# Kernel tuning notes

Hardware: AMD Instinct MI355X
Metric: run time of the kernel (lower is better)

The kernel has to match this reference:

```python
import jax, jax.numpy as jnp
import numpy as np

K = 5      # kernel_size
STRIDE = 1
EPS = 1e-7


def _extract_patches(x, k, s):
    # x: [B,H,W,C] -> [B,Ho,Wo,k,k,C], same (kh,kw,c) layout as tf.extract_image_patches VALID
    B, H, W, C = x.shape
    Ho = (H - k) // s + 1
    Wo = (W - k) // s + 1
    r = (jnp.arange(Ho) * s)[:, None] + jnp.arange(k)   # [Ho,k]
    c = (jnp.arange(Wo) * s)[:, None] + jnp.arange(k)   # [Wo,k]
    return x[:, r[:, None, :, None], c[None, :, None, :], :]


def _rotate(pflat, angle, k):
    # Replicates tf.contrib.image.transform with angles_to_projective_transforms,
    # including the (1+1e-7) normalization of the 3x3 matrix in the original code.
    # pflat: [N, k*k, C], angle: [N]; bilinear sampling, fill value 0 outside.
    N = pflat.shape[0]
    f32 = pflat.dtype
    co, si = jnp.cos(angle), jnp.sin(angle)
    km1 = jnp.asarray(k - 1, f32)
    xoff = (km1 - (co * km1 - si * km1)) * 0.5
    yoff = (km1 - (si * km1 + co * km1)) * 0.5
    scale = 1.0 / (1.0 + EPS)  # transforms /= transforms[:, 8:9] + 1e-7
    gy, gx = jnp.meshgrid(jnp.arange(k, dtype=f32), jnp.arange(k, dtype=f32), indexing='ij')
    sx = (co[:, None, None] * gx - si[:, None, None] * gy + xoff[:, None, None]) * scale
    sy = (si[:, None, None] * gx + co[:, None, None] * gy + yoff[:, None, None]) * scale
    sx = sx.reshape(N, k * k)
    sy = sy.reshape(N, k * k)
    x0 = jnp.floor(sx)
    y0 = jnp.floor(sy)
    wx = (sx - x0)[..., None]
    wy = (sy - y0)[..., None]
    x0i = x0.astype(jnp.int32)
    y0i = y0.astype(jnp.int32)

    def samp(yi, xi):
        valid = (xi >= 0) & (xi < k) & (yi >= 0) & (yi < k)
        idx = jnp.clip(yi, 0, k - 1) * k + jnp.clip(xi, 0, k - 1)   # [N,k*k]
        v = jnp.take_along_axis(pflat, idx[..., None], axis=1)      # [N,k*k,C]
        return jnp.where(valid[..., None], v, jnp.zeros((), f32))

    v00 = samp(y0i, x0i)
    v01 = samp(y0i, x0i + 1)
    v10 = samp(y0i + 1, x0i)
    v11 = samp(y0i + 1, x0i + 1)
    top = v00 * (1 - wx) + v01 * wx
    bot = v10 * (1 - wx) + v11 * wx
    return top * (1 - wy) + bot * wy   # [N,k*k,C]


def _forward(input_tensor, W, b):
    k, s = K, STRIDE
    B, H, Wd, C = input_tensor.shape
    patches = _extract_patches(input_tensor, k, s)      # [B,Ho,Wo,k,k,C]
    Ho, Wo = patches.shape[1], patches.shape[2]
    inten = patches.sum(-1)                             # [B,Ho,Wo,k,k] channel-sum intensity
    ridx = jnp.arange(k, dtype=patches.dtype)
    tot = inten.sum((-2, -1)) + EPS
    cr = (inten * ridx[:, None]).sum((-2, -1)) / tot    # centroid row
    cc = (inten * ridx[None, :]).sum((-2, -1)) / tot    # centroid col
    m = (k - 1) / 2.0                                   # meanCenter (same for row/col)
    angle = jnp.arctan2(cr - m, cc - m + EPS)           # [B,Ho,Wo]
    pflat = patches.reshape(B * Ho * Wo, k * k, C)
    rot = _rotate(pflat, angle.reshape(-1), k)          # [N,k*k,C]
    rot = rot.reshape(B, Ho * Wo, k * k * C)
    wflat = W.reshape(W.shape[0], -1)                   # [F, k*k*C]
    out = jnp.einsum('bpd,fd->bpf', rot, wflat)         # elementwise-mult-sum 'conv'
    return out.reshape(B, Ho, Wo, -1) + b


def setup_inputs():
    key = jax.random.key(0)
    k1, k2 = jax.random.split(key, 2)
    B, H, Wd, C, F = 4, 128, 128, 16, 32
    input_tensor = jax.random.uniform(k1, (B, H, Wd, C), dtype=jnp.float32)
    lim = float(np.sqrt(6.0 / (K * K * C + F)))  # glorot_uniform
    W = jax.random.uniform(k2, (F, K, K, C), minval=-lim, maxval=lim, dtype=jnp.float32)
    b = jnp.zeros((F,), jnp.float32)
    return {"input_tensor": input_tensor, "W": W, "b": b}


def reference(input_tensor, W, b):
    return _forward(input_tensor, W, b)
```

## Files before the change

### kernel.cpp

```cpp
#include <hip/hip_runtime.h>


#define KS     5
#define TILE   8
#define NPIX   64
#define TW     (TILE + KS - 1)
#define CPAD   20
#define C_IN   16
#define F_OUT  32
#define H_IN   128
#define W_IN   128
#define HO     124
#define WO     124
#define NBATCH 4
#define EPSF   1e-7f
#define BLOCK  256
#define NCHUNK 7
#define AROW   72
#define KW     400

typedef __attribute__((ext_vector_type(8))) short  short8;
typedef __attribute__((ext_vector_type(4))) float  floatx4;

static __device__ __forceinline__ short f2bf(float f) {
    union { float f; unsigned u; } v; v.f = f;
    unsigned r = v.u + 0x7fffu + ((v.u >> 16) & 1u);
    return (short)(r >> 16);
}

__global__ __launch_bounds__(BLOCK) void rotconv_kernel(
    const float* __restrict__ in, const float* __restrict__ Wg,
    const float* __restrict__ bg, float* __restrict__ out)
{
    __shared__ float s_in[TW * TW * CPAD];
    __shared__ float s_int[TW * (TW + 1)];
    __shared__ short sA[NPIX * AROW];

    const int tid  = threadIdx.x;
    const int bx = blockIdx.x, by = blockIdx.y, bimg = blockIdx.z;
    const int ox = bx * TILE, oy = by * TILE;

    const float* inb = in + (size_t)bimg * (H_IN * W_IN * C_IN);
    for (int i = tid; i < TW * TW * (C_IN / 4); i += BLOCK) {
        int cv = i & 3;
        int pp = i >> 2;
        int x = pp % TW, y = pp / TW;
        int gy = oy + y, gx = ox + x;
        float4 v = make_float4(0.f, 0.f, 0.f, 0.f);
        if (gy < H_IN && gx < W_IN)
            v = *(const float4*)(inb + ((size_t)(gy * W_IN + gx) * C_IN) + 4 * cv);
        *(float4*)(&s_in[pp * CPAD + 4 * cv]) = v;
    }
    __syncthreads();

    for (int pp = tid; pp < TW * TW; pp += BLOCK) {
        const float* sp = &s_in[pp * CPAD];
        float s = 0.f;
        #pragma unroll
        for (int c = 0; c < C_IN; ++c) s += sp[c];
        s_int[(pp / TW) * (TW + 1) + (pp % TW)] = s;
    }
    __syncthreads();

    const int p    = tid & 63;
    const int wv   = tid >> 6;
    const int lx   = p & 7, ly = p >> 3;
    const int col  = p & 15;
    const int quad = p >> 4;

    float tot = EPSF, cr = 0.f, cc = 0.f;
    #pragma unroll
    for (int dy = 0; dy < KS; ++dy)
        #pragma unroll
        for (int dx = 0; dx < KS; ++dx) {
            float v = s_int[(ly + dy) * (TW + 1) + (lx + dx)];
            tot += v; cr += v * (float)dy; cc += v * (float)dx;
        }
    cr /= tot; cc /= tot;
    float ang = atan2f(cr - 2.0f, cc - 2.0f + EPSF);
    float si, co;
    sincosf(ang, &si, &co);
    const float scl = 1.0f / (1.0f + EPSF);
    float xoff = (4.0f - (co * 4.0f - si * 4.0f)) * 0.5f;
    float yoff = (4.0f - (si * 4.0f + co * 4.0f)) * 0.5f;

    const int nt  = wv >> 1;
    const int mt0 = (wv & 1) * 2;

    floatx4 acc0, acc1;
    {
        float bv = bg[nt * 16 + col];
        acc0 = (floatx4){bv, bv, bv, bv};
        acc1 = acc0;
    }

    for (int ch = 0; ch < NCHUNK; ++ch) {
        int t = 4 * ch + wv;
        short8 alo = {0,0,0,0,0,0,0,0}, ahi = {0,0,0,0,0,0,0,0};
        if (t < KS * KS) {
            int ky = t / KS, kx = t - KS * ky;
            float sx = (co * (float)kx - si * (float)ky + xoff) * scl;
            float sy = (si * (float)kx + co * (float)ky + yoff) * scl;
            float fx0 = floorf(sx), fy0 = floorf(sy);
            float wx = sx - fx0, wy = sy - fy0;
            int x0 = (int)fx0, y0 = (int)fy0;
            int x1 = x0 + 1, y1 = y0 + 1;
            float vx0 = (x0 >= 0 && x0 < KS) ? 1.f : 0.f;
            float vx1 = (x1 >= 0 && x1 < KS) ? 1.f : 0.f;
            float vy0 = (y0 >= 0 && y0 < KS) ? 1.f : 0.f;
            float vy1 = (y1 >= 0 && y1 < KS) ? 1.f : 0.f;
            float w00 = (1.f - wx) * (1.f - wy) * vx0 * vy0;
            float w01 = wx * (1.f - wy) * vx1 * vy0;
            float w10 = (1.f - wx) * wy * vx0 * vy1;
            float w11 = wx * wy * vx1 * vy1;
            int cx0 = min(max(x0, 0), KS - 1), cx1 = min(max(x1, 0), KS - 1);
            int cy0 = min(max(y0, 0), KS - 1), cy1 = min(max(y1, 0), KS - 1);
            const float* p00 = &s_in[((ly + cy0) * TW + (lx + cx0)) * CPAD];
            const float* p01 = &s_in[((ly + cy0) * TW + (lx + cx1)) * CPAD];
            const float* p10 = &s_in[((ly + cy1) * TW + (lx + cx0)) * CPAD];
            const float* p11 = &s_in[((ly + cy1) * TW + (lx + cx1)) * CPAD];
            float r[16];
            #pragma unroll
            for (int cv = 0; cv < 4; ++cv) {
                float4 a = *(const float4*)(p00 + 4 * cv);
                float4 b = *(const float4*)(p01 + 4 * cv);
                float4 c = *(const float4*)(p10 + 4 * cv);
                float4 d = *(const float4*)(p11 + 4 * cv);
                r[4*cv+0] = w00 * a.x + w01 * b.x + w10 * c.x + w11 * d.x;
                r[4*cv+1] = w00 * a.y + w01 * b.y + w10 * c.y + w11 * d.y;
                r[4*cv+2] = w00 * a.z + w01 * b.z + w10 * c.z + w11 * d.z;
                r[4*cv+3] = w00 * a.w + w01 * b.w + w10 * c.w + w11 * d.w;
            }
            alo = (short8){f2bf(r[0]), f2bf(r[1]), f2bf(r[2]), f2bf(r[3]),
                           f2bf(r[4]), f2bf(r[5]), f2bf(r[6]), f2bf(r[7])};
            ahi = (short8){f2bf(r[8]),  f2bf(r[9]),  f2bf(r[10]), f2bf(r[11]),
                           f2bf(r[12]), f2bf(r[13]), f2bf(r[14]), f2bf(r[15])};
        }
        __syncthreads();
        *(short8*)(&sA[p * AROW + wv * 16])     = alo;
        *(short8*)(&sA[p * AROW + wv * 16 + 8]) = ahi;
        __syncthreads();

        int nk = (ch == NCHUNK - 1) ? 1 : 2;
        for (int kk = 0; kk < nk; ++kk) {
            int kg = ch * 64 + kk * 32 + quad * 8;
            short8 bf = {0,0,0,0,0,0,0,0};
            if (kg + 8 <= KW) {
                const float* wp = Wg + (size_t)(nt * 16 + col) * KW + kg;
                float4 a = *(const float4*)(wp);
                float4 b = *(const float4*)(wp + 4);
                bf = (short8){f2bf(a.x), f2bf(a.y), f2bf(a.z), f2bf(a.w),
                              f2bf(b.x), f2bf(b.y), f2bf(b.z), f2bf(b.w)};
            }
            short8 a0 = *(const short8*)(&sA[(16 * mt0 + col) * AROW + kk * 32 + quad * 8]);
            short8 a1 = *(const short8*)(&sA[(16 * mt0 + 16 + col) * AROW + kk * 32 + quad * 8]);
            acc0 = __builtin_amdgcn_mfma_f32_16x16x32_bf16(a0, bf, acc0, 0, 0, 0);
            acc1 = __builtin_amdgcn_mfma_f32_16x16x32_bf16(a1, bf, acc1, 0, 0, 0);
        }
    }

    #pragma unroll
    for (int r = 0; r < 4; ++r) {
        int pix0 = 16 * mt0 + quad * 4 + r;
        int ho = oy + (pix0 >> 3), wo = ox + (pix0 & 7);
        if (ho < HO && wo < WO)
            out[(((size_t)bimg * HO + ho) * WO + wo) * F_OUT + nt * 16 + col] = acc0[r];
        int pix1 = pix0 + 16;
        ho = oy + (pix1 >> 3); wo = ox + (pix1 & 7);
        if (ho < HO && wo < WO)
            out[(((size_t)bimg * HO + ho) * WO + wo) * F_OUT + nt * 16 + col] = acc1[r];
    }
}

extern "C" void kernel_launch(void* const* d_in, const int* in_sizes, int n_in,
                              void* d_out, int out_size, void* d_ws, size_t ws_size,
                              hipStream_t stream) {
    const float* in = (const float*)d_in[0];
    const float* Wg = (const float*)d_in[1];
    const float* bg = (const float*)d_in[2];
    float* out      = (float*)d_out;
    dim3 grid((WO + TILE - 1) / TILE, (HO + TILE - 1) / TILE, NBATCH);
    rotconv_kernel<<<grid, dim3(BLOCK), 0, stream>>>(in, Wg, bg, out);
}
```

Before: 75.94 us.

## Split K across waves with register-built A fragments and LDS reduction

Each wave now handles a subset of the 25 kernel taps for all 64 pixels and both filter halves, building bf16 A fragments directly in registers by bilinear blending instead of staging them through shared memory. Per-pixel angles are computed once by one wave and shared. Partial accumulators from the four waves are reduced through LDS and written with vectorized float4 stores. This removes the per-chunk double barriers and the sA staging, but adds a cross-wave reduction, more accumulator registers, and some redundant blend work. The launch-bounds hint now requests two blocks per CU.

New measurement: 74.09 us. 1.02x faster.

```diff
diff --git a/kernel.cpp b/kernel.cpp
--- a/kernel.cpp
+++ b/kernel.cpp
@@ -3,7 +3,6 @@
 
 #define KS     5
 #define TILE   8
-#define NPIX   64
 #define TW     (TILE + KS - 1)
 #define CPAD   20
 #define C_IN   16
@@ -15,9 +14,12 @@
 #define NBATCH 4
 #define EPSF   1e-7f
 #define BLOCK  256
-#define NCHUNK 7
-#define AROW   72
 #define KW     400
+
+#define ANG_OFF     12160
+#define RED_STRIDE  34
+#define RED_WAVE    (64 * RED_STRIDE)
+#define SMEM_BYTES  34816
 
 typedef __attribute__((ext_vector_type(8))) short  short8;
 typedef __attribute__((ext_vector_type(4))) float  floatx4;
@@ -28,13 +30,57 @@
     return (short)(r >> 16);
 }
 
-__global__ __launch_bounds__(BLOCK) void rotconv_kernel(
+static __device__ __forceinline__ short8 blend8(
+    const float* __restrict__ s_in, int lxq, int lyq,
+    float co, float si, float xo, float yo, int t, int ch0)
+{
+    const float scl = 1.0f / (1.0f + EPSF);
+    int ky = t / KS, kx = t - KS * ky;
+    float sx = (co * (float)kx - si * (float)ky + xo) * scl;
+    float sy = (si * (float)kx + co * (float)ky + yo) * scl;
+    float fx0 = floorf(sx), fy0 = floorf(sy);
+    float wx = sx - fx0, wy = sy - fy0;
+    int x0 = (int)fx0, y0 = (int)fy0;
+    int x1 = x0 + 1, y1 = y0 + 1;
+    float vx0 = (x0 >= 0 && x0 < KS) ? 1.f : 0.f;
+    float vx1 = (x1 >= 0 && x1 < KS) ? 1.f : 0.f;
+    float vy0 = (y0 >= 0 && y0 < KS) ? 1.f : 0.f;
+    float vy1 = (y1 >= 0 && y1 < KS) ? 1.f : 0.f;
+    float w00 = (1.f - wx) * (1.f - wy) * vx0 * vy0;
+    float w01 = wx * (1.f - wy) * vx1 * vy0;
+    float w10 = (1.f - wx) * wy * vx0 * vy1;
+    float w11 = wx * wy * vx1 * vy1;
+    int cx0 = min(max(x0, 0), KS - 1), cx1 = min(max(x1, 0), KS - 1);
+    int cy0 = min(max(y0, 0), KS - 1), cy1 = min(max(y1, 0), KS - 1);
+    const float* p00 = &s_in[((lyq + cy0) * TW + (lxq + cx0)) * CPAD + ch0];
+    const float* p01 = &s_in[((lyq + cy0) * TW + (lxq + cx1)) * CPAD + ch0];
+    const float* p10 = &s_in[((lyq + cy1) * TW + (lxq + cx0)) * CPAD + ch0];
+    const float* p11 = &s_in[((lyq + cy1) * TW + (lxq + cx1)) * CPAD + ch0];
+    float r[8];
+    #pragma unroll
+    for (int cv = 0; cv < 2; ++cv) {
+        float4 a = *(const float4*)(p00 + 4 * cv);
+        float4 b = *(const float4*)(p01 + 4 * cv);
+        float4 c = *(const float4*)(p10 + 4 * cv);
+        float4 d = *(const float4*)(p11 + 4 * cv);
+        r[4*cv+0] = w00 * a.x + w01 * b.x + w10 * c.x + w11 * d.x;
+        r[4*cv+1] = w00 * a.y + w01 * b.y + w10 * c.y + w11 * d.y;
+        r[4*cv+2] = w00 * a.z + w01 * b.z + w10 * c.z + w11 * d.z;
+        r[4*cv+3] = w00 * a.w + w01 * b.w + w10 * c.w + w11 * d.w;
+    }
+    return (short8){f2bf(r[0]), f2bf(r[1]), f2bf(r[2]), f2bf(r[3]),
+                    f2bf(r[4]), f2bf(r[5]), f2bf(r[6]), f2bf(r[7])};
+}
+
+__global__ __launch_bounds__(BLOCK, 2) void rotconv_kernel(
     const float* __restrict__ in, const float* __restrict__ Wg,
     const float* __restrict__ bg, float* __restrict__ out)
 {
-    __shared__ float s_in[TW * TW * CPAD];
-    __shared__ float s_int[TW * (TW + 1)];
-    __shared__ short sA[NPIX * AROW];
+    __shared__ __align__(16) char smem[SMEM_BYTES];
+    float*  s_in   = (float*)smem;
+    float*  s_int  = (float*)(smem + 11520);
+    float4* s_ang4 = (float4*)(smem + ANG_OFF);
+    float*  red    = (float*)smem;
 
     const int tid  = threadIdx.x;
     const int bx = blockIdx.x, by = blockIdx.y, bimg = blockIdx.z;
@@ -62,113 +108,109 @@
     }
     __syncthreads();
 
+    if (tid < 64) {
+        const int alx = tid & 7, aly = tid >> 3;
+        float tot = EPSF, cr = 0.f, cc = 0.f;
+        #pragma unroll
+        for (int dy = 0; dy < KS; ++dy)
+            #pragma unroll
+            for (int dx = 0; dx < KS; ++dx) {
+                float v = s_int[(aly + dy) * (TW + 1) + (alx + dx)];
+                tot += v; cr += v * (float)dy; cc += v * (float)dx;
+            }
+        cr /= tot; cc /= tot;
+        float ang = atan2f(cr - 2.0f, cc - 2.0f + EPSF);
+        float si, co;
+        sincosf(ang, &si, &co);
+        float xoff = (4.0f - (co * 4.0f - si * 4.0f)) * 0.5f;
+        float yoff = (4.0f - (si * 4.0f + co * 4.0f)) * 0.5f;
+        s_ang4[tid] = make_float4(co, si, xoff, yoff);
+    }
+    __syncthreads();
+
     const int p    = tid & 63;
     const int wv   = tid >> 6;
-    const int lx   = p & 7, ly = p >> 3;
     const int col  = p & 15;
     const int quad = p >> 4;
 
-    float tot = EPSF, cr = 0.f, cc = 0.f;
-    #pragma unroll
-    for (int dy = 0; dy < KS; ++dy)
-        #pragma unroll
-        for (int dx = 0; dx < KS; ++dx) {
-            float v = s_int[(ly + dy) * (TW + 1) + (lx + dx)];
-            tot += v; cr += v * (float)dy; cc += v * (float)dx;
+    float4 angs[4];
+    #pragma unroll
+    for (int m = 0; m < 4; ++m) angs[m] = s_ang4[16 * m + col];
+
+    floatx4 acc[4][2];
+    #pragma unroll
+    for (int m = 0; m < 4; ++m) {
+        acc[m][0] = (floatx4){0.f, 0.f, 0.f, 0.f};
+        acc[m][1] = acc[m][0];
+    }
+
+    const int nstep = (wv == 0) ? 4 : 3;
+    const int lxq = col & 7, lyq0 = col >> 3;
+    const int ch0 = (quad & 1) * 8;
+    const short8 zero8 = {0,0,0,0,0,0,0,0};
+
+    #pragma unroll
+    for (int s = 0; s < 4; ++s) {
+        if (s < nstep) {
+            const int ta = wv + 8 * s;
+            const int tb = ta + 4;
+            const int tq = (quad < 2) ? ta : tb;
+
+            short8 bf0 = zero8, bf1 = zero8;
+            if (tq < KS * KS) {
+                const float* wp0 = Wg + (size_t)col * KW + tq * 16 + ch0;
+                float4 a = *(const float4*)(wp0);
+                float4 b = *(const float4*)(wp0 + 4);
+                bf0 = (short8){f2bf(a.x), f2bf(a.y), f2bf(a.z), f2bf(a.w),
+                               f2bf(b.x), f2bf(b.y), f2bf(b.z), f2bf(b.w)};
+                const float* wp1 = wp0 + (size_t)16 * KW;
+                float4 c = *(const float4*)(wp1);
+                float4 d = *(const float4*)(wp1 + 4);
+                bf1 = (short8){f2bf(c.x), f2bf(c.y), f2bf(c.z), f2bf(c.w),
+                               f2bf(d.x), f2bf(d.y), f2bf(d.z), f2bf(d.w)};
+            }
+
+            #pragma unroll
+            for (int m = 0; m < 4; ++m) {
+                short8 av = zero8;
+                if (tq < KS * KS)
+                    av = blend8(s_in, lxq, 2 * m + lyq0,
+                                angs[m].x, angs[m].y, angs[m].z, angs[m].w,
+                                tq, ch0);
+                acc[m][0] = __builtin_amdgcn_mfma_f32_16x16x32_bf16(av, bf0, acc[m][0], 0, 0, 0);
+                acc[m][1] = __builtin_amdgcn_mfma_f32_16x16x32_bf16(av, bf1, acc[m][1], 0, 0, 0);
+            }
         }
-    cr /= tot; cc /= tot;
-    float ang = atan2f(cr - 2.0f, cc - 2.0f + EPSF);
-    float si, co;
-    sincosf(ang, &si, &co);
-    const float scl = 1.0f / (1.0f + EPSF);
-    float xoff = (4.0f - (co * 4.0f - si * 4.0f)) * 0.5f;
-    float yoff = (4.0f - (si * 4.0f + co * 4.0f)) * 0.5f;
-
-    const int nt  = wv >> 1;
-    const int mt0 = (wv & 1) * 2;
-
-    floatx4 acc0, acc1;
-    {
-        float bv = bg[nt * 16 + col];
-        acc0 = (floatx4){bv, bv, bv, bv};
-        acc1 = acc0;
-    }
-
-    for (int ch = 0; ch < NCHUNK; ++ch) {
-        int t = 4 * ch + wv;
-        short8 alo = {0,0,0,0,0,0,0,0}, ahi = {0,0,0,0,0,0,0,0};
-        if (t < KS * KS) {
-            int ky = t / KS, kx = t - KS * ky;
-            float sx = (co * (float)kx - si * (float)ky + xoff) * scl;
-            float sy = (si * (float)kx + co * (float)ky + yoff) * scl;
-            float fx0 = floorf(sx), fy0 = floorf(sy);
-            float wx = sx - fx0, wy = sy - fy0;
-            int x0 = (int)fx0, y0 = (int)fy0;
-            int x1 = x0 + 1, y1 = y0 + 1;
-            float vx0 = (x0 >= 0 && x0 < KS) ? 1.f : 0.f;
-            float vx1 = (x1 >= 0 && x1 < KS) ? 1.f : 0.f;
-            float vy0 = (y0 >= 0 && y0 < KS) ? 1.f : 0.f;
-            float vy1 = (y1 >= 0 && y1 < KS) ? 1.f : 0.f;
-            float w00 = (1.f - wx) * (1.f - wy) * vx0 * vy0;
-            float w01 = wx * (1.f - wy) * vx1 * vy0;
-            float w10 = (1.f - wx) * wy * vx0 * vy1;
-            float w11 = wx * wy * vx1 * vy1;
-            int cx0 = min(max(x0, 0), KS - 1), cx1 = min(max(x1, 0), KS - 1);
-            int cy0 = min(max(y0, 0), KS - 1), cy1 = min(max(y1, 0), KS - 1);
-            const float* p00 = &s_in[((ly + cy0) * TW + (lx + cx0)) * CPAD];
-            const float* p01 = &s_in[((ly + cy0) * TW + (lx + cx1)) * CPAD];
-            const float* p10 = &s_in[((ly + cy1) * TW + (lx + cx0)) * CPAD];
-            const float* p11 = &s_in[((ly + cy1) * TW + (lx + cx1)) * CPAD];
-            float r[16];
+    }
+
+    __syncthreads();
+    #pragma unroll
+    for (int m = 0; m < 4; ++m)
+        #pragma unroll
+        for (int n = 0; n < 2; ++n)
             #pragma unroll
-            for (int cv = 0; cv < 4; ++cv) {
-                float4 a = *(const float4*)(p00 + 4 * cv);
-                float4 b = *(const float4*)(p01 + 4 * cv);
-                float4 c = *(const float4*)(p10 + 4 * cv);
-                float4 d = *(const float4*)(p11 + 4 * cv);
-                r[4*cv+0] = w00 * a.x + w01 * b.x + w10 * c.x + w11 * d.x;
-                r[4*cv+1] = w00 * a.y + w01 * b.y + w10 * c.y + w11 * d.y;
-                r[4*cv+2] = w00 * a.z + w01 * b.z + w10 * c.z + w11 * d.z;
-                r[4*cv+3] = w00 * a.w + w01 * b.w + w10 * c.w + w11 * d.w;
-            }
-            alo = (short8){f2bf(r[0]), f2bf(r[1]), f2bf(r[2]), f2bf(r[3]),
-                           f2bf(r[4]), f2bf(r[5]), f2bf(r[6]), f2bf(r[7])};
-            ahi = (short8){f2bf(r[8]),  f2bf(r[9]),  f2bf(r[10]), f2bf(r[11]),
-                           f2bf(r[12]), f2bf(r[13]), f2bf(r[14]), f2bf(r[15])};
-        }
-        __syncthreads();
-        *(short8*)(&sA[p * AROW + wv * 16])     = alo;
-        *(short8*)(&sA[p * AROW + wv * 16 + 8]) = ahi;
-        __syncthreads();
-
-        int nk = (ch == NCHUNK - 1) ? 1 : 2;
-        for (int kk = 0; kk < nk; ++kk) {
-            int kg = ch * 64 + kk * 32 + quad * 8;
-            short8 bf = {0,0,0,0,0,0,0,0};
-            if (kg + 8 <= KW) {
-                const float* wp = Wg + (size_t)(nt * 16 + col) * KW + kg;
-                float4 a = *(const float4*)(wp);
-                float4 b = *(const float4*)(wp + 4);
-                bf = (short8){f2bf(a.x), f2bf(a.y), f2bf(a.z), f2bf(a.w),
-                              f2bf(b.x), f2bf(b.y), f2bf(b.z), f2bf(b.w)};
-            }
-            short8 a0 = *(const short8*)(&sA[(16 * mt0 + col) * AROW + kk * 32 + quad * 8]);
-            short8 a1 = *(const short8*)(&sA[(16 * mt0 + 16 + col) * AROW + kk * 32 + quad * 8]);
-            acc0 = __builtin_amdgcn_mfma_f32_16x16x32_bf16(a0, bf, acc0, 0, 0, 0);
-            acc1 = __builtin_amdgcn_mfma_f32_16x16x32_bf16(a1, bf, acc1, 0, 0, 0);
-        }
-    }
-
-    #pragma unroll
-    for (int r = 0; r < 4; ++r) {
-        int pix0 = 16 * mt0 + quad * 4 + r;
-        int ho = oy + (pix0 >> 3), wo = ox + (pix0 & 7);
-        if (ho < HO && wo < WO)
-            out[(((size_t)bimg * HO + ho) * WO + wo) * F_OUT + nt * 16 + col] = acc0[r];
-        int pix1 = pix0 + 16;
-        ho = oy + (pix1 >> 3); wo = ox + (pix1 & 7);
-        if (ho < HO && wo < WO)
-            out[(((size_t)bimg * HO + ho) * WO + wo) * F_OUT + nt * 16 + col] = acc1[r];
+            for (int r = 0; r < 4; ++r) {
+                int px = 16 * m + 4 * quad + r;
+                red[wv * RED_WAVE + px * RED_STRIDE + n * 16 + col] = acc[m][n][r];
+            }
+    __syncthreads();
+
+    const int rpx = tid >> 2;
+    const int rf0 = (tid & 3) * 8;
+    float sum[8];
+    #pragma unroll
+    for (int j = 0; j < 8; ++j) sum[j] = bg[rf0 + j];
+    #pragma unroll
+    for (int w = 0; w < 4; ++w) {
+        const float* rp = red + w * RED_WAVE + rpx * RED_STRIDE + rf0;
+        #pragma unroll
+        for (int j = 0; j < 8; ++j) sum[j] += rp[j];
+    }
+    const int ho = oy + (rpx >> 3), wo = ox + (rpx & 7);
+    if (ho < HO && wo < WO) {
+        float* op = out + (((size_t)bimg * HO + ho) * WO + wo) * F_OUT + rf0;
+        *(float4*)op       = make_float4(sum[0], sum[1], sum[2], sum[3]);
+        *(float4*)(op + 4) = make_float4(sum[4], sum[5], sum[6], sum[7]);
     }
 }
 
```
